# Optimization experiments

Hardware: AMD Instinct MI355X
Metric: run time of the kernel (lower is better)

Reference implementation:

```python
import jax, jax.numpy as jnp
import numpy as np

EPS = 1e-5
CHUNK = 256
N_LAYERS = 4
D_MODEL = 1024
D_INNER = 2048
D_HEAD = 64
N_HEADS = 32
D_STATE = 64
D_CONV = 4
CONV_DIM = D_INNER + 2 * D_STATE  # ngroups=1
D_IN_PROJ = 2 * D_INNER + 2 * D_STATE + N_HEADS


def silu(x):
    return x * jax.nn.sigmoid(x)


def rmsnorm(x, w):
    return x * jax.lax.rsqrt(jnp.mean(x * x, axis=-1, keepdims=True) + EPS) * w


def segsum(x):
    # x: [..., T] -> [..., T, T] lower-triangular segment sums, -inf above diag
    T = x.shape[-1]
    cs = jnp.cumsum(x, axis=-1)
    ss = cs[..., :, None] - cs[..., None, :]
    mask = jnp.tril(jnp.ones((T, T), dtype=bool))
    return jnp.where(mask, ss, -jnp.inf)


def ssd(X, A, B, C, chunk):
    # X: [b,l,h,p] (already scaled by dt), A: [b,l,h] (= dt * A_head), B,C: [b,l,n] (ngroups=1)
    b, l, h, p = X.shape
    c = l // chunk
    X = X.reshape(b, c, chunk, h, p)
    A = A.reshape(b, c, chunk, h).transpose(0, 3, 1, 2)  # [b,h,c,l]
    B = B.reshape(b, c, chunk, -1)
    C = C.reshape(b, c, chunk, -1)
    Acs = jnp.cumsum(A, axis=-1)  # [b,h,c,l]
    # intra-chunk (diagonal blocks)
    Lm = jnp.exp(segsum(A))  # [b,h,c,l,l]
    Y_diag = jnp.einsum('bcln,bcsn,bhcls,bcshp->bclhp', C, B, Lm, X)
    # chunk end states
    decay_states = jnp.exp(Acs[..., -1:] - Acs)  # [b,h,c,l]
    states = jnp.einsum('bcln,bhcl,bclhp->bchpn', B, decay_states, X)
    # inter-chunk recurrence (c is small -> dense segsum over chunks)
    A_last = jnp.pad(Acs[..., -1], ((0, 0), (0, 0), (1, 0)))  # [b,h,c+1]
    decay_chunk = jnp.exp(segsum(A_last))  # [b,h,c+1,c+1]
    states = jnp.concatenate([jnp.zeros_like(states[:, :1]), states], axis=1)
    new_states = jnp.einsum('bhzc,bchpn->bzhpn', decay_chunk, states)
    states = new_states[:, :-1]  # state entering each chunk
    Y_off = jnp.einsum('bcln,bchpn,bhcl->bclhp', C, states, jnp.exp(Acs))
    return (Y_diag + Y_off).reshape(b, l, h, p)


def mamba2_layer(x, in_w, conv_w, conv_b, dt_bias, A_log, D, gnorm_w, out_w):
    b, l, _ = x.shape
    zxbcdt = jnp.einsum('bld,ed->ble', x, in_w)  # [b,l,D_IN_PROJ]
    z = zxbcdt[..., :D_INNER]
    xBC = zxbcdt[..., D_INNER:D_INNER + CONV_DIM]
    dt = zxbcdt[..., D_INNER + CONV_DIM:]  # [b,l,h]
    # depthwise causal conv1d + silu
    xpad = jnp.pad(xBC, ((0, 0), (D_CONV - 1, 0), (0, 0)))
    xconv = conv_b
    for k in range(D_CONV):
        xconv = xconv + xpad[:, k:k + l, :] * conv_w[:, k]
    xBC = silu(xconv)
    x_in = xBC[..., :D_INNER]
    B = xBC[..., D_INNER:D_INNER + D_STATE]
    C = xBC[..., D_INNER + D_STATE:]
    dt = jax.nn.softplus(dt + dt_bias)  # [b,l,h]
    A = -jnp.exp(A_log)  # [h]
    X = x_in.reshape(b, l, N_HEADS, D_HEAD)
    y = ssd(X * dt[..., None], dt * A, B, C, CHUNK)
    y = y + D[None, None, :, None] * X
    y = y.reshape(b, l, D_INNER)
    y = rmsnorm(y * silu(z), gnorm_w)
    return jnp.einsum('ble,de->bld', y, out_w)


def setup_inputs() -> dict:
    key = jax.random.key(0)
    ks = jax.random.split(key, 8)
    x = jax.random.normal(ks[0], (2, 2048, D_MODEL), dtype=jnp.float32)
    in_proj_w = jax.random.normal(ks[1], (N_LAYERS, D_IN_PROJ, D_MODEL), dtype=jnp.float32) * 0.02
    conv_w = jax.random.uniform(ks[2], (N_LAYERS, CONV_DIM, D_CONV), dtype=jnp.float32, minval=-0.5, maxval=0.5)
    conv_b = jnp.zeros((N_LAYERS, CONV_DIM), dtype=jnp.float32)
    A_log = jnp.log(jax.random.uniform(ks[3], (N_LAYERS, N_HEADS), dtype=jnp.float32, minval=1.0, maxval=16.0))
    dt0 = jax.random.uniform(ks[4], (N_LAYERS, N_HEADS), dtype=jnp.float32, minval=0.001, maxval=0.1)
    dt_bias = dt0 + jnp.log(-jnp.expm1(-dt0))  # inverse softplus
    D = jnp.ones((N_LAYERS, N_HEADS), dtype=jnp.float32)
    gnorm_w = jnp.ones((N_LAYERS, D_INNER), dtype=jnp.float32)
    out_proj_w = jax.random.normal(ks[5], (N_LAYERS, D_MODEL, D_INNER), dtype=jnp.float32) * 0.02
    rms_w = jnp.ones((N_LAYERS, D_MODEL), dtype=jnp.float32)
    return {"x": x, "in_proj_w": in_proj_w, "conv_w": conv_w, "conv_b": conv_b,
            "dt_bias": dt_bias, "A_log": A_log, "D": D, "gnorm_w": gnorm_w,
            "out_proj_w": out_proj_w, "rms_w": rms_w}


def reference(x, in_proj_w, conv_w, conv_b, dt_bias, A_log, D, gnorm_w, out_proj_w, rms_w):
    for i in range(N_LAYERS):
        x = x + mamba2_layer(rmsnorm(x, rms_w[i]), in_proj_w[i], conv_w[i], conv_b[i],
                             dt_bias[i], A_log[i], D[i], gnorm_w[i], out_proj_w[i])
    return x
```

## Files before the change

### kernel.cpp

```cpp
#include <hip/hip_runtime.h>
#include <cmath>

#define BATCH 2
#define LSEQ 2048
#define DMODEL 1024
#define DINNER 2048
#define NHEADS 32
#define DHEAD 64
#define DSTATE 64
#define DCONV 4
#define CONVDIM (DINNER + 2*DSTATE)
#define DINPROJ (2*DINNER + 2*DSTATE + NHEADS)
#define DINPROJ_PAD 4352
#define CHUNKSZ 256
#define NCHUNK (LSEQ/CHUNKSZ)
#define MROWS (BATCH*LSEQ)
#define EPSF 1e-5f

typedef __attribute__((ext_vector_type(8))) short shortx8;
typedef __attribute__((ext_vector_type(4))) short shortx4;
typedef __attribute__((ext_vector_type(4))) float floatx4;

__device__ __forceinline__ ushort f2bf(float f) {
  unsigned u = __float_as_uint(f);
  unsigned r = (u + 0x7fffu + ((u >> 16) & 1u)) >> 16;
  return (ushort)r;
}
__device__ __forceinline__ float bf2f(ushort b) {
  return __uint_as_float(((unsigned)b) << 16);
}

__device__ __forceinline__ shortx8 pack8(float4 a, float4 b) {
  shortx8 r;
  r[0] = (short)f2bf(a.x); r[1] = (short)f2bf(a.y);
  r[2] = (short)f2bf(a.z); r[3] = (short)f2bf(a.w);
  r[4] = (short)f2bf(b.x); r[5] = (short)f2bf(b.y);
  r[6] = (short)f2bf(b.z); r[7] = (short)f2bf(b.w);
  return r;
}

__device__ __forceinline__ void async_load16(const void* g, void* l) {
  __builtin_amdgcn_global_load_lds(
      (const __attribute__((address_space(1))) void*)g,
      (__attribute__((address_space(3))) void*)l, 16, 0, 0);
}

__device__ __forceinline__ float block_reduce_sum_256(float v, float* sb) {
  for (int off = 32; off > 0; off >>= 1) v += __shfl_down(v, off, 64);
  int lane = threadIdx.x & 63, wid = threadIdx.x >> 6;
  if (lane == 0) sb[wid] = v;
  __syncthreads();
  return sb[0] + sb[1] + sb[2] + sb[3];
}

__global__ __launch_bounds__(256) void cvt_bf16_k(const float* __restrict__ src,
                                                  ushort* __restrict__ dst,
                                                  size_t n_src, size_t n_dst) {
  size_t i = (size_t)blockIdx.x * 256 + threadIdx.x;
  if (i >= n_dst) return;
  float v = (i < n_src) ? src[i] : 0.f;
  dst[i] = f2bf(v);
}

__global__ __launch_bounds__(256) void rmsnorm_k(const float* __restrict__ x,
                                                 const float* __restrict__ w,
                                                 ushort* __restrict__ out) {
  __shared__ float sb[4];
  int r = blockIdx.x;
  const float* xr = x + (size_t)r * DMODEL;
  ushort* orow = out + (size_t)r * DMODEL;
  float v[4]; float ssq = 0.f;
  for (int i = 0; i < 4; i++) {
    v[i] = xr[threadIdx.x + i * 256];
    ssq += v[i] * v[i];
  }
  float s = block_reduce_sum_256(ssq, sb);
  float sc = rsqrtf(s / (float)DMODEL + EPSF);
  for (int i = 0; i < 4; i++) {
    int c = threadIdx.x + i * 256;
    orow[c] = f2bf(v[i] * sc * w[c]);
  }
}

__device__ __forceinline__ void stage_tile(const ushort* __restrict__ A,
                                           const ushort* __restrict__ B,
                                           char* lb, int m0, int n0, int K, int k0,
                                           int wid, int rA, int sA) {
#pragma unroll
  for (int rd = 0; rd < 2; rd++) {
    int r = rd * 64 + rA;
    int sl = sA ^ ((r ^ (r >> 2)) & 3);
    async_load16(A + (size_t)(m0 + r) * K + (k0 + sl * 8), lb + rd * 4096 + wid * 1024);
  }
#pragma unroll
  for (int rd = 0; rd < 2; rd++) {
    int r = rd * 64 + rA;
    int sl = sA ^ ((r ^ (r >> 2)) & 3);
    async_load16(B + (size_t)(n0 + r) * K + (k0 + sl * 8), lb + 8192 + rd * 4096 + wid * 1024);
  }
}

template <int CFG>
__global__ __launch_bounds__(256, CFG == 0 ? 3 : 2) void gemm_nt_mfma_pipe(
    const ushort* __restrict__ A, const ushort* __restrict__ B,
    float* __restrict__ C, ushort* __restrict__ Cbf,
    const float* __restrict__ resid, int M, int N, int K,
    int nbx, int rw, int rh) {
  constexpr int NBUF = (CFG == 0) ? 3 : 5;
  __shared__ __align__(16) char lds[NBUF][16384];
  int tid = threadIdx.x;
  int wid = tid >> 6, lane = tid & 63;
  int quad = lane >> 4, lrow = lane & 15;

  int d = blockIdx.x;
  int xcd = d & 7, wi = d >> 3;
  int ra = nbx / rw;
  int rn = xcd % ra, rm = xcd / ra;
  int bx = rn * rw + wi % rw;
  int by = rm * rh + wi / rw;

  int m0 = by * 128, n0 = bx * 128;
  int wm = (wid >> 1) * 64, wn = (wid & 1) * 64;
  int rA = tid >> 2, sA = tid & 3;

  floatx4 acc[4][4];
#pragma unroll
  for (int i = 0; i < 4; i++)
#pragma unroll
    for (int j = 0; j < 4; j++) acc[i][j] = (floatx4){0.f, 0.f, 0.f, 0.f};

  int NT = K >> 5;
  constexpr int DEPTH = (CFG == 0) ? 2 : 3;
#pragma unroll
  for (int t = 0; t < DEPTH; t++)
    stage_tile(A, B, lds[t], m0, n0, K, t * 32, wid, rA, sA);

  int cur = 0, sb = DEPTH;
  for (int t = 0; t < NT; t++) {
    if (CFG == 1) {
      __builtin_amdgcn_sched_barrier(0);
      if (t + 3 < NT) {
        stage_tile(A, B, lds[sb], m0, n0, K, (t + 3) * 32, wid, rA, sA);
        sb = (sb == NBUF - 1) ? 0 : sb + 1;
      }
      int rem = NT - 1 - t;
      if (rem >= 3)      asm volatile("s_waitcnt vmcnt(12)" ::: "memory");
      else if (rem == 2) asm volatile("s_waitcnt vmcnt(8)" ::: "memory");
      else if (rem == 1) asm volatile("s_waitcnt vmcnt(4)" ::: "memory");
      else               asm volatile("s_waitcnt vmcnt(0)" ::: "memory");
      __builtin_amdgcn_s_barrier();
      __builtin_amdgcn_sched_barrier(0);
    } else {
      if (t < NT - 1) asm volatile("s_waitcnt vmcnt(4)" ::: "memory");
      else            asm volatile("s_waitcnt vmcnt(0)" ::: "memory");
      __builtin_amdgcn_s_barrier();
      __builtin_amdgcn_sched_barrier(0);
      if (t + 2 < NT) {
        stage_tile(A, B, lds[sb], m0, n0, K, (t + 2) * 32, wid, rA, sA);
        sb = (sb == NBUF - 1) ? 0 : sb + 1;
      }
    }

    const char* Ab = lds[cur];
    const char* Bb = Ab + 8192;
    cur = (cur == NBUF - 1) ? 0 : cur + 1;
    shortx8 af[4], bfr[4];
#pragma unroll
    for (int i = 0; i < 4; i++) {
      int r = wm + i * 16 + lrow;
      af[i] = *(const shortx8*)(Ab + r * 64 + ((quad ^ ((r ^ (r >> 2)) & 3)) << 4));
    }
#pragma unroll
    for (int j = 0; j < 4; j++) {
      int r = wn + j * 16 + lrow;
      bfr[j] = *(const shortx8*)(Bb + r * 64 + ((quad ^ ((r ^ (r >> 2)) & 3)) << 4));
    }
    __builtin_amdgcn_s_setprio(1);
#pragma unroll
    for (int i = 0; i < 4; i++)
#pragma unroll
      for (int j = 0; j < 4; j++)
        acc[i][j] = __builtin_amdgcn_mfma_f32_16x16x32_bf16(af[i], bfr[j], acc[i][j], 0, 0, 0);
    __builtin_amdgcn_s_setprio(0);
  }

  if (Cbf) {
#pragma unroll
    for (int i = 0; i < 4; i++) {
      int r0 = m0 + wm + i * 16 + quad * 4;
#pragma unroll
      for (int j = 0; j < 4; j++) {
        int n = n0 + wn + j * 16 + lrow;
        if (n < N)
#pragma unroll
          for (int r = 0; r < 4; r++)
            Cbf[(size_t)(r0 + r) * N + n] = f2bf(acc[i][j][r]);
      }
    }
  } else {
    bool hasR = (resid != nullptr);
#pragma unroll
    for (int i = 0; i < 4; i++) {
      int r0 = m0 + wm + i * 16 + quad * 4;
#pragma unroll
      for (int j = 0; j < 4; j++) {
        int n = n0 + wn + j * 16 + lrow;
        if (n < N) {
#pragma unroll
          for (int r = 0; r < 4; r++) {
            size_t idx = (size_t)(r0 + r) * N + n;
            float v = acc[i][j][r];
            if (hasR) v += resid[idx];
            C[idx] = v;
          }
        }
      }
    }
  }
}

__global__ __launch_bounds__(256) void conv_silu_v2(const ushort* __restrict__ zxbf,
                                                    const float* __restrict__ cw,
                                                    const float* __restrict__ cb,
                                                    ushort* __restrict__ xbf) {
  int r0 = blockIdx.x * 8;
  int bstart = r0 & ~(LSEQ - 1);
  int tid = threadIdx.x;
#pragma unroll
  for (int rep = 0; rep < 2; rep++) {
    int ch;
    if (rep == 0) ch = tid * 8;
    else { if (tid >= (CONVDIM - 2048) / 8) break; ch = 2048 + tid * 8; }
    float wv[8][4], bias[8];
#pragma unroll
    for (int j = 0; j < 8; j++) {
      float4 w4 = *(const float4*)(cw + (ch + j) * 4);
      wv[j][0] = w4.x; wv[j][1] = w4.y; wv[j][2] = w4.z; wv[j][3] = w4.w;
      bias[j] = cb[ch + j];
    }
    float xw[11][8];
#pragma unroll
    for (int wr = 0; wr < 11; wr++) {
      int rr = r0 - 3 + wr;
      if (rr < bstart) {
#pragma unroll
        for (int j = 0; j < 8; j++) xw[wr][j] = 0.f;
      } else {
        shortx8 v = *(const shortx8*)(zxbf + (size_t)rr * DINPROJ + DINNER + ch);
#pragma unroll
        for (int j = 0; j < 8; j++) xw[wr][j] = bf2f((ushort)v[j]);
      }
    }
#pragma unroll
    for (int o = 0; o < 8; o++) {
      shortx8 ov;
#pragma unroll
      for (int j = 0; j < 8; j++) {
        float acc = bias[j];
#pragma unroll
        for (int k = 0; k < 4; k++) acc += xw[o + k][j] * wv[j][k];
        float s = acc / (1.f + expf(-acc));
        ov[j] = (short)f2bf(s);
      }
      *(shortx8*)(xbf + (size_t)(r0 + o) * CONVDIM + ch) = ov;
    }
  }
}

__global__ __launch_bounds__(256) void cumsum_k(const ushort* __restrict__ zxbf,
                                                const float* __restrict__ dt_bias,
                                                const float* __restrict__ A_log,
                                                float* __restrict__ dt_sp,
                                                float* __restrict__ dtA_cs) {
  __shared__ float buf[256];
  int bid = blockIdx.x;
  int h = bid & 31, c = (bid >> 5) & 7, b = bid >> 8;
  int l = threadIdx.x;
  float Aneg = -expf(A_log[h]);
  int row = b * LSEQ + c * CHUNKSZ + l;
  float v = bf2f(zxbf[(size_t)row * DINPROJ + DINNER + CONVDIM + h]) + dt_bias[h];
  float dtv = (v > 20.f) ? v : log1pf(expf(v));
  dt_sp[row * 32 + h] = dtv;
  buf[l] = dtv * Aneg;
  __syncthreads();
  for (int off = 1; off < 256; off <<= 1) {
    float add = (l >= off) ? buf[l - off] : 0.f;
    __syncthreads();
    buf[l] += add;
    __syncthreads();
  }
  dtA_cs[(size_t)bid * CHUNKSZ + l] = buf[l];
}

#define ST_STRIDE 72
__global__ __launch_bounds__(256) void states_mfma(const ushort* __restrict__ xbf,
                                                   const float* __restrict__ dt_sp,
                                                   const float* __restrict__ dtA_cs,
                                                   float* __restrict__ st_raw) {
  __shared__ ushort XT[64 * ST_STRIDE];
  __shared__ ushort BT[64 * ST_STRIDE];
  __shared__ float wrow[64];
  int bid = blockIdx.x;
  int h = bid & 31, c = (bid >> 5) & 7, b = bid >> 8;
  int tid = threadIdx.x;
  int w = tid >> 6, lane = tid & 63;
  int quad = lane >> 4, lrow = lane & 15;
  int cbase = bid * CHUNKSZ;
  int rowbase = b * LSEQ + c * CHUNKSZ;
  float T = dtA_cs[cbase + CHUNKSZ - 1];
  floatx4 acc[4];
  for (int jt = 0; jt < 4; jt++) acc[jt] = (floatx4){0.f, 0.f, 0.f, 0.f};
  int half = tid & 31, srb = tid >> 5;
  for (int lt = 0; lt < 4; lt++) {
    __syncthreads();
    if (tid < 64) {
      int row = rowbase + lt * 64 + tid;
      wrow[tid] = dt_sp[row * 32 + h] * __expf(T - dtA_cs[cbase + lt * 64 + tid]);
    }
    __syncthreads();
    for (int pass = 0; pass < 8; pass++) {
      int sr = srb + pass * 8;
      int row = rowbase + lt * 64 + sr;
      uint bv = *(const uint*)(xbf + (size_t)row * CONVDIM + DINNER + 2 * half);
      uint xv = *(const uint*)(xbf + (size_t)row * CONVDIM + h * DHEAD + 2 * half);
      float wv = wrow[sr];
      BT[(2 * half) * ST_STRIDE + sr]     = (ushort)(bv & 0xffff);
      BT[(2 * half + 1) * ST_STRIDE + sr] = (ushort)(bv >> 16);
      XT[(2 * half) * ST_STRIDE + sr]     = f2bf(bf2f((ushort)(xv & 0xffff)) * wv);
      XT[(2 * half + 1) * ST_STRIDE + sr] = f2bf(bf2f((ushort)(xv >> 16)) * wv);
    }
    __syncthreads();
    for (int kk = 0; kk < 64; kk += 32) {
      shortx8 af = *(const shortx8*)&XT[(w * 16 + lrow) * ST_STRIDE + kk + quad * 8];
      for (int jt = 0; jt < 4; jt++) {
        shortx8 bf = *(const shortx8*)&BT[(jt * 16 + lrow) * ST_STRIDE + kk + quad * 8];
        acc[jt] = __builtin_amdgcn_mfma_f32_16x16x32_bf16(af, bf, acc[jt], 0, 0, 0);
      }
    }
  }
  size_t base = (size_t)bid * (DHEAD * DSTATE);
  for (int jt = 0; jt < 4; jt++) {
    int n = jt * 16 + lrow;
    for (int r = 0; r < 4; r++) {
      int p = w * 16 + quad * 4 + r;
      st_raw[base + (size_t)p * 64 + n] = acc[jt][r];
    }
  }
}

__global__ __launch_bounds__(256) void scan_k(float* __restrict__ st,
                                              const float* __restrict__ dtA_cs) {
  int bid = blockIdx.x;
  int seg = bid & 3, h = (bid >> 2) & 31, b = bid >> 7;
  int tid = threadIdx.x;
  int off = seg * 1024;
  float s[4];
  for (int i = 0; i < 4; i++) s[i] = 0.f;
  for (int c = 0; c < NCHUNK; c++) {
    int g = (b * NCHUNK + c) * 32 + h;
    float dec = expf(dtA_cs[(size_t)g * CHUNKSZ + CHUNKSZ - 1]);
    size_t base = (size_t)g * (DHEAD * DSTATE) + off;
    for (int i = 0; i < 4; i++) {
      int idx = tid + i * 256;
      float raw = st[base + idx];
      st[base + idx] = s[i];
      s[i] = s[i] * dec + raw;
    }
  }
}

#define BS_STRIDE 72
#define XT_STRIDE 68
#define PW_STRIDE 72
__global__ __launch_bounds__(256) void ydiag_mfma(const ushort* __restrict__ xbf,
                                                  const float* __restrict__ dt_sp,
                                                  const float* __restrict__ dtA_cs,
                                                  const float* __restrict__ st_in,
                                                  ushort* __restrict__ Y) {
  __shared__ ushort Bs[64 * BS_STRIDE];
  __shared__ ushort XsT[64 * XT_STRIDE];
  __shared__ ushort Pw[4 * 16 * PW_STRIDE];
  __shared__ float cs[256];
  int tid = threadIdx.x;
  int w = tid >> 6, lane = tid & 63;
  int quad = lane >> 4, lrow = lane & 15;
  int bid = blockIdx.x;
  int lt = bid & 3, h = (bid >> 2) & 31, c = (bid >> 7) & 7, b = bid >> 10;
  int g = (b * NCHUNK + c) * 32 + h;
  int cbase = g * CHUNKSZ;
  int rowbase = b * LSEQ + c * CHUNKSZ;

  cs[tid] = dtA_cs[cbase + tid];
  __syncthreads();

  int mrow = lt * 64 + w * 16;
  float csl[4];
  for (int r = 0; r < 4; r++) csl[r] = cs[mrow + quad * 4 + r];

  shortx8 Cf[2];
  {
    const ushort* cp = xbf + (size_t)(rowbase + mrow + lrow) * CONVDIM + DINNER + DSTATE;
    for (int q = 0; q < 2; q++)
      Cf[q] = *(const shortx8*)(cp + q * 32 + quad * 8);
  }

  floatx4 acc[4];
  for (int jt = 0; jt < 4; jt++) acc[jt] = (floatx4){0.f, 0.f, 0.f, 0.f};
  const float* stp = st_in + (size_t)g * (DHEAD * DSTATE);
  for (int q = 0; q < 2; q++) {
    for (int jt = 0; jt < 4; jt++) {
      const float* sp = stp + (size_t)(jt * 16 + lrow) * 64 + q * 32 + quad * 8;
      shortx8 sf = pack8(*(const float4*)sp, *(const float4*)(sp + 4));
      acc[jt] = __builtin_amdgcn_mfma_f32_16x16x32_bf16(Cf[q], sf, acc[jt], 0, 0, 0);
    }
  }
  for (int jt = 0; jt < 4; jt++)
    for (int r = 0; r < 4; r++) acc[jt][r] *= __expf(csl[r]);

  ushort* myP = Pw + w * 16 * PW_STRIDE;
  int half = tid & 31, srb = tid >> 5;
  for (int st = 0; st <= lt; st++) {
    __syncthreads();
    for (int pass = 0; pass < 8; pass++) {
      int sr = srb + pass * 8;
      int row = rowbase + st * 64 + sr;
      uint bv = *(const uint*)(xbf + (size_t)row * CONVDIM + DINNER + 2 * half);
      *(uint*)&Bs[sr * BS_STRIDE + 2 * half] = bv;
      float dtv = dt_sp[row * 32 + h];
      uint xv = *(const uint*)(xbf + (size_t)row * CONVDIM + h * DHEAD + 2 * half);
      XsT[(2 * half) * XT_STRIDE + sr]     = f2bf(bf2f((ushort)(xv & 0xffff)) * dtv);
      XsT[(2 * half + 1) * XT_STRIDE + sr] = f2bf(bf2f((ushort)(xv >> 16)) * dtv);
    }
    __syncthreads();
    for (int jt = 0; jt < 4; jt++) {
      floatx4 s = (floatx4){0.f, 0.f, 0.f, 0.f};
      for (int q = 0; q < 2; q++) {
        shortx8 bfr = *(const shortx8*)&Bs[(jt * 16 + lrow) * BS_STRIDE + q * 32 + quad * 8];
        s = __builtin_amdgcn_mfma_f32_16x16x32_bf16(Cf[q], bfr, s, 0, 0, 0);
      }
      int scol = st * 64 + jt * 16 + lrow;
      float css = cs[scol];
      for (int r = 0; r < 4; r++) {
        int l = mrow + quad * 4 + r;
        float v = (scol <= l) ? s[r] * __expf(csl[r] - css) : 0.f;
        myP[(quad * 4 + r) * PW_STRIDE + jt * 16 + lrow] = f2bf(v);
      }
    }
    shortx8 pf[2];
    for (int q = 0; q < 2; q++)
      pf[q] = *(const shortx8*)&myP[lrow * PW_STRIDE + q * 32 + quad * 8];
    for (int jt = 0; jt < 4; jt++) {
      for (int q = 0; q < 2; q++) {
        const ushort* xp = &XsT[(jt * 16 + lrow) * XT_STRIDE + q * 32 + quad * 8];
        shortx4 lo = *(const shortx4*)xp;
        shortx4 hi = *(const shortx4*)(xp + 4);
        shortx8 xf = __builtin_shufflevector(lo, hi, 0, 1, 2, 3, 4, 5, 6, 7);
        acc[jt] = __builtin_amdgcn_mfma_f32_16x16x32_bf16(pf[q], xf, acc[jt], 0, 0, 0);
      }
    }
  }
  int growb = rowbase + mrow + quad * 4;
  for (int jt = 0; jt < 4; jt++)
    for (int r = 0; r < 4; r++)
      Y[(size_t)(growb + r) * DINNER + h * DHEAD + jt * 16 + lrow] = f2bf(acc[jt][r]);
}

__global__ __launch_bounds__(256) void gatenorm_k(const ushort* __restrict__ Ybf,
                                                  const ushort* __restrict__ zxbf,
                                                  const ushort* __restrict__ xbf,
                                                  const float* __restrict__ Dvec,
                                                  const float* __restrict__ gw,
                                                  ushort* __restrict__ obf) {
  __shared__ float sb[4];
  int r = blockIdx.x;
  const ushort* yr = Ybf + (size_t)r * DINNER;
  const ushort* zr = zxbf + (size_t)r * DINPROJ;
  const ushort* xr = xbf + (size_t)r * CONVDIM;
  ushort* orow = obf + (size_t)r * DINNER;
  float t[8]; float ssq = 0.f;
  for (int i = 0; i < 8; i++) {
    int cc = threadIdx.x + i * 256;
    float z = bf2f(zr[cc]);
    float yv = bf2f(yr[cc]) + Dvec[cc >> 6] * bf2f(xr[cc]);
    float gv = yv * (z / (1.f + expf(-z)));
    t[i] = gv;
    ssq += gv * gv;
  }
  float s = block_reduce_sum_256(ssq, sb);
  float sc = rsqrtf(s / (float)DINNER + EPSF);
  for (int i = 0; i < 8; i++) {
    int cc = threadIdx.x + i * 256;
    orow[cc] = f2bf(t[i] * sc * gw[cc]);
  }
}

extern "C" void kernel_launch(void* const* d_in, const int* in_sizes, int n_in,
                              void* d_out, int out_size, void* d_ws, size_t ws_size,
                              hipStream_t stream) {
  const float* x_in     = (const float*)d_in[0];
  const float* in_w     = (const float*)d_in[1];
  const float* conv_w   = (const float*)d_in[2];
  const float* conv_b   = (const float*)d_in[3];
  const float* dt_bias  = (const float*)d_in[4];
  const float* A_log    = (const float*)d_in[5];
  const float* Dvec     = (const float*)d_in[6];
  const float* gnorm_w  = (const float*)d_in[7];
  const float* out_w    = (const float*)d_in[8];
  const float* rms_w    = (const float*)d_in[9];
  float* out = (float*)d_out;

  float* ws = (float*)d_ws;
  size_t o = 0;
  float* x_cur  = ws + o; o += (size_t)MROWS * DMODEL;
  ushort* zx_bf = (ushort*)(ws + o); o += (size_t)MROWS * DINPROJ / 2;
  ushort* xbf   = (ushort*)(ws + o); o += (size_t)MROWS * CONVDIM / 2;
  float* dt_sp  = ws + o; o += (size_t)MROWS * NHEADS;
  float* dtA_cs = ws + o; o += (size_t)BATCH * NCHUNK * NHEADS * CHUNKSZ;
  float* st     = ws + o; o += (size_t)BATCH * NCHUNK * NHEADS * DHEAD * DSTATE;
  ushort* Ybf   = (ushort*)(ws + o); o += (size_t)MROWS * DINNER / 2;
  ushort* act_bf = (ushort*)(ws + o); o += (size_t)MROWS * DINNER / 2;
  ushort* w_bf   = (ushort*)(ws + o); o += (size_t)DINPROJ_PAD * DMODEL / 2;

  hipMemcpyAsync(x_cur, x_in, (size_t)MROWS * DMODEL * sizeof(float),
                 hipMemcpyDeviceToDevice, stream);

  for (int i = 0; i < 4; i++) {
    const float* in_w_i   = in_w    + (size_t)i * DINPROJ * DMODEL;
    const float* conv_w_i = conv_w  + (size_t)i * CONVDIM * DCONV;
    const float* conv_b_i = conv_b  + (size_t)i * CONVDIM;
    const float* dtb_i    = dt_bias + (size_t)i * NHEADS;
    const float* Alog_i   = A_log   + (size_t)i * NHEADS;
    const float* D_i      = Dvec    + (size_t)i * NHEADS;
    const float* gw_i     = gnorm_w + (size_t)i * DINNER;
    const float* out_w_i  = out_w   + (size_t)i * DMODEL * DINNER;
    const float* rms_w_i  = rms_w   + (size_t)i * DMODEL;

    {
      size_t ns = (size_t)DINPROJ * DMODEL, nd = (size_t)DINPROJ_PAD * DMODEL;
      cvt_bf16_k<<<(nd + 255) / 256, 256, 0, stream>>>(in_w_i, w_bf, ns, nd);
    }
    rmsnorm_k<<<MROWS, 256, 0, stream>>>(x_cur, rms_w_i, act_bf);
    gemm_nt_mfma_pipe<0><<<(DINPROJ_PAD / 128) * (MROWS / 128), 256, 0, stream>>>(
        act_bf, w_bf, nullptr, zx_bf, nullptr, MROWS, DINPROJ, DMODEL,
        DINPROJ_PAD / 128, 17, 8);
    conv_silu_v2<<<MROWS / 8, 256, 0, stream>>>(zx_bf, conv_w_i, conv_b_i, xbf);
    cumsum_k<<<BATCH * NCHUNK * NHEADS, 256, 0, stream>>>(zx_bf, dtb_i, Alog_i, dt_sp, dtA_cs);
    states_mfma<<<BATCH * NCHUNK * NHEADS, 256, 0, stream>>>(xbf, dt_sp, dtA_cs, st);
    scan_k<<<BATCH * NHEADS * 4, 256, 0, stream>>>(st, dtA_cs);
    ydiag_mfma<<<BATCH * NCHUNK * NHEADS * 4, 256, 0, stream>>>(
        xbf, dt_sp, dtA_cs, st, Ybf);
    gatenorm_k<<<MROWS, 256, 0, stream>>>(Ybf, zx_bf, xbf, D_i, gw_i, act_bf);
    {
      size_t ns = (size_t)DMODEL * DINNER;
      cvt_bf16_k<<<(ns + 255) / 256, 256, 0, stream>>>(out_w_i, w_bf, ns, ns);
    }
    float* outC = (i == 3) ? out : x_cur;
    gemm_nt_mfma_pipe<1><<<(DMODEL / 128) * (MROWS / 128), 256, 0, stream>>>(
        act_bf, w_bf, outC, nullptr, x_cur, MROWS, DMODEL, DINNER,
        DMODEL / 128, 4, 8);
  }
}
```

Baseline: 984.2 us.

## Hoist weight conversion, merge conv and cumsum, swizzle states LDS, vectorize norms

All per-layer in_proj and out_proj weights are converted to bf16 in one launch up front when the workspace is large enough, replacing eight per-layer conversion kernels with one. The conv+silu and dt cumsum kernels are merged into a single launch whose blocks split by index. The states kernel's LDS transpose now uses an XOR swizzle to reduce bank conflicts. The rmsnorm and gatenorm kernels switch to contiguous vectorized loads and stores. The hoisted path needs extra workspace and falls back to the old per-layer conversion if the workspace is too small.

```diff
diff --git a/kernel.cpp b/kernel.cpp
--- a/kernel.cpp
+++ b/kernel.cpp
@@ -62,6 +62,27 @@
   dst[i] = f2bf(v);
 }
 
+__global__ __launch_bounds__(256) void cvt_w_all(const float* __restrict__ in_w,
+                                                 const float* __restrict__ out_w,
+                                                 ushort* __restrict__ in_bf,
+                                                 ushort* __restrict__ out_bf) {
+  unsigned i = blockIdx.x * 256u + threadIdx.x;
+  const unsigned PL = (unsigned)DINPROJ_PAD * DMODEL;
+  const unsigned n1 = 4u * PL;
+  const unsigned n2 = 4u * DMODEL * DINNER;
+  if (i < n1) {
+    unsigned layer = i / PL, rem = i % PL;
+    unsigned row = rem / DMODEL, col = rem % DMODEL;
+    float v = (row < DINPROJ)
+                  ? in_w[((size_t)layer * DINPROJ + row) * DMODEL + col]
+                  : 0.f;
+    in_bf[i] = f2bf(v);
+  } else if (i < n1 + n2) {
+    unsigned j = i - n1;
+    out_bf[j] = f2bf(out_w[j]);
+  }
+}
+
 __global__ __launch_bounds__(256) void rmsnorm_k(const float* __restrict__ x,
                                                  const float* __restrict__ w,
                                                  ushort* __restrict__ out) {
@@ -69,17 +90,18 @@
   int r = blockIdx.x;
   const float* xr = x + (size_t)r * DMODEL;
   ushort* orow = out + (size_t)r * DMODEL;
-  float v[4]; float ssq = 0.f;
-  for (int i = 0; i < 4; i++) {
-    v[i] = xr[threadIdx.x + i * 256];
-    ssq += v[i] * v[i];
-  }
+  int c0 = threadIdx.x * 4;
+  float4 v4 = *(const float4*)(xr + c0);
+  float ssq = v4.x * v4.x + v4.y * v4.y + v4.z * v4.z + v4.w * v4.w;
   float s = block_reduce_sum_256(ssq, sb);
   float sc = rsqrtf(s / (float)DMODEL + EPSF);
-  for (int i = 0; i < 4; i++) {
-    int c = threadIdx.x + i * 256;
-    orow[c] = f2bf(v[i] * sc * w[c]);
-  }
+  float4 w4 = *(const float4*)(w + c0);
+  shortx4 o;
+  o[0] = (short)f2bf(v4.x * sc * w4.x);
+  o[1] = (short)f2bf(v4.y * sc * w4.y);
+  o[2] = (short)f2bf(v4.z * sc * w4.z);
+  o[3] = (short)f2bf(v4.w * sc * w4.w);
+  *(shortx4*)(orow + c0) = o;
 }
 
 __device__ __forceinline__ void stage_tile(const ushort* __restrict__ A,
@@ -219,77 +241,77 @@
   }
 }
 
-__global__ __launch_bounds__(256) void conv_silu_v2(const ushort* __restrict__ zxbf,
-                                                    const float* __restrict__ cw,
-                                                    const float* __restrict__ cb,
-                                                    ushort* __restrict__ xbf) {
-  int r0 = blockIdx.x * 8;
-  int bstart = r0 & ~(LSEQ - 1);
+__global__ __launch_bounds__(256) void convcum_k(const ushort* __restrict__ zxbf,
+                                                 const float* __restrict__ cw,
+                                                 const float* __restrict__ cb,
+                                                 ushort* __restrict__ xbf,
+                                                 const float* __restrict__ dt_bias,
+                                                 const float* __restrict__ A_log,
+                                                 float* __restrict__ dt_sp,
+                                                 float* __restrict__ dtA_cs) {
+  __shared__ float buf[256];
   int tid = threadIdx.x;
-#pragma unroll
-  for (int rep = 0; rep < 2; rep++) {
-    int ch;
-    if (rep == 0) ch = tid * 8;
-    else { if (tid >= (CONVDIM - 2048) / 8) break; ch = 2048 + tid * 8; }
-    float wv[8][4], bias[8];
-#pragma unroll
-    for (int j = 0; j < 8; j++) {
-      float4 w4 = *(const float4*)(cw + (ch + j) * 4);
-      wv[j][0] = w4.x; wv[j][1] = w4.y; wv[j][2] = w4.z; wv[j][3] = w4.w;
-      bias[j] = cb[ch + j];
-    }
-    float xw[11][8];
-#pragma unroll
-    for (int wr = 0; wr < 11; wr++) {
-      int rr = r0 - 3 + wr;
-      if (rr < bstart) {
-#pragma unroll
-        for (int j = 0; j < 8; j++) xw[wr][j] = 0.f;
-      } else {
-        shortx8 v = *(const shortx8*)(zxbf + (size_t)rr * DINPROJ + DINNER + ch);
-#pragma unroll
-        for (int j = 0; j < 8; j++) xw[wr][j] = bf2f((ushort)v[j]);
-      }
-    }
-#pragma unroll
-    for (int o = 0; o < 8; o++) {
-      shortx8 ov;
+  if (blockIdx.x < MROWS / 8) {
+    int r0 = blockIdx.x * 8;
+    int bstart = r0 & ~(LSEQ - 1);
+#pragma unroll
+    for (int rep = 0; rep < 2; rep++) {
+      int ch;
+      if (rep == 0) ch = tid * 8;
+      else { if (tid >= (CONVDIM - 2048) / 8) break; ch = 2048 + tid * 8; }
+      float wv[8][4], bias[8];
 #pragma unroll
       for (int j = 0; j < 8; j++) {
-        float acc = bias[j];
-#pragma unroll
-        for (int k = 0; k < 4; k++) acc += xw[o + k][j] * wv[j][k];
-        float s = acc / (1.f + expf(-acc));
-        ov[j] = (short)f2bf(s);
-      }
-      *(shortx8*)(xbf + (size_t)(r0 + o) * CONVDIM + ch) = ov;
-    }
-  }
-}
-
-__global__ __launch_bounds__(256) void cumsum_k(const ushort* __restrict__ zxbf,
-                                                const float* __restrict__ dt_bias,
-                                                const float* __restrict__ A_log,
-                                                float* __restrict__ dt_sp,
-                                                float* __restrict__ dtA_cs) {
-  __shared__ float buf[256];
-  int bid = blockIdx.x;
-  int h = bid & 31, c = (bid >> 5) & 7, b = bid >> 8;
-  int l = threadIdx.x;
-  float Aneg = -expf(A_log[h]);
-  int row = b * LSEQ + c * CHUNKSZ + l;
-  float v = bf2f(zxbf[(size_t)row * DINPROJ + DINNER + CONVDIM + h]) + dt_bias[h];
-  float dtv = (v > 20.f) ? v : log1pf(expf(v));
-  dt_sp[row * 32 + h] = dtv;
-  buf[l] = dtv * Aneg;
-  __syncthreads();
-  for (int off = 1; off < 256; off <<= 1) {
-    float add = (l >= off) ? buf[l - off] : 0.f;
+        float4 w4 = *(const float4*)(cw + (ch + j) * 4);
+        wv[j][0] = w4.x; wv[j][1] = w4.y; wv[j][2] = w4.z; wv[j][3] = w4.w;
+        bias[j] = cb[ch + j];
+      }
+      float xw[11][8];
+#pragma unroll
+      for (int wr = 0; wr < 11; wr++) {
+        int rr = r0 - 3 + wr;
+        if (rr < bstart) {
+#pragma unroll
+          for (int j = 0; j < 8; j++) xw[wr][j] = 0.f;
+        } else {
+          shortx8 v = *(const shortx8*)(zxbf + (size_t)rr * DINPROJ + DINNER + ch);
+#pragma unroll
+          for (int j = 0; j < 8; j++) xw[wr][j] = bf2f((ushort)v[j]);
+        }
+      }
+#pragma unroll
+      for (int o = 0; o < 8; o++) {
+        shortx8 ov;
+#pragma unroll
+        for (int j = 0; j < 8; j++) {
+          float acc = bias[j];
+#pragma unroll
+          for (int k = 0; k < 4; k++) acc += xw[o + k][j] * wv[j][k];
+          float s = acc / (1.f + expf(-acc));
+          ov[j] = (short)f2bf(s);
+        }
+        *(shortx8*)(xbf + (size_t)(r0 + o) * CONVDIM + ch) = ov;
+      }
+    }
+  } else {
+    int bid = blockIdx.x - MROWS / 8;
+    int h = bid & 31, c = (bid >> 5) & 7, b = bid >> 8;
+    int l = tid;
+    float Aneg = -expf(A_log[h]);
+    int row = b * LSEQ + c * CHUNKSZ + l;
+    float v = bf2f(zxbf[(size_t)row * DINPROJ + DINNER + CONVDIM + h]) + dt_bias[h];
+    float dtv = (v > 20.f) ? v : log1pf(expf(v));
+    dt_sp[row * 32 + h] = dtv;
+    buf[l] = dtv * Aneg;
     __syncthreads();
-    buf[l] += add;
-    __syncthreads();
-  }
-  dtA_cs[(size_t)bid * CHUNKSZ + l] = buf[l];
+    for (int off = 1; off < 256; off <<= 1) {
+      float add = (l >= off) ? buf[l - off] : 0.f;
+      __syncthreads();
+      buf[l] += add;
+      __syncthreads();
+    }
+    dtA_cs[(size_t)bid * CHUNKSZ + l] = buf[l];
+  }
 }
 
 #define ST_STRIDE 72
@@ -311,6 +333,7 @@
   floatx4 acc[4];
   for (int jt = 0; jt < 4; jt++) acc[jt] = (floatx4){0.f, 0.f, 0.f, 0.f};
   int half = tid & 31, srb = tid >> 5;
+  int ekey = (half & 7) << 3;
   for (int lt = 0; lt < 4; lt++) {
     __syncthreads();
     if (tid < 64) {
@@ -324,16 +347,21 @@
       uint bv = *(const uint*)(xbf + (size_t)row * CONVDIM + DINNER + 2 * half);
       uint xv = *(const uint*)(xbf + (size_t)row * CONVDIM + h * DHEAD + 2 * half);
       float wv = wrow[sr];
-      BT[(2 * half) * ST_STRIDE + sr]     = (ushort)(bv & 0xffff);
-      BT[(2 * half + 1) * ST_STRIDE + sr] = (ushort)(bv >> 16);
-      XT[(2 * half) * ST_STRIDE + sr]     = f2bf(bf2f((ushort)(xv & 0xffff)) * wv);
-      XT[(2 * half + 1) * ST_STRIDE + sr] = f2bf(bf2f((ushort)(xv >> 16)) * wv);
+      int sc = sr ^ ekey;
+      BT[(2 * half) * ST_STRIDE + sc]     = (ushort)(bv & 0xffff);
+      BT[(2 * half + 1) * ST_STRIDE + sc] = (ushort)(bv >> 16);
+      XT[(2 * half) * ST_STRIDE + sc]     = f2bf(bf2f((ushort)(xv & 0xffff)) * wv);
+      XT[(2 * half + 1) * ST_STRIDE + sc] = f2bf(bf2f((ushort)(xv >> 16)) * wv);
     }
     __syncthreads();
+    int arow = w * 16 + lrow;
+    int akey = ((arow >> 1) & 7) << 3;
     for (int kk = 0; kk < 64; kk += 32) {
-      shortx8 af = *(const shortx8*)&XT[(w * 16 + lrow) * ST_STRIDE + kk + quad * 8];
+      shortx8 af = *(const shortx8*)&XT[arow * ST_STRIDE + ((kk + quad * 8) ^ akey)];
       for (int jt = 0; jt < 4; jt++) {
-        shortx8 bf = *(const shortx8*)&BT[(jt * 16 + lrow) * ST_STRIDE + kk + quad * 8];
+        int brow = jt * 16 + lrow;
+        int bkey = ((brow >> 1) & 7) << 3;
+        shortx8 bf = *(const shortx8*)&BT[brow * ST_STRIDE + ((kk + quad * 8) ^ bkey)];
         acc[jt] = __builtin_amdgcn_mfma_f32_16x16x32_bf16(af, bf, acc[jt], 0, 0, 0);
       }
     }
@@ -473,25 +501,34 @@
                                                   ushort* __restrict__ obf) {
   __shared__ float sb[4];
   int r = blockIdx.x;
+  int c0 = threadIdx.x * 8;
   const ushort* yr = Ybf + (size_t)r * DINNER;
   const ushort* zr = zxbf + (size_t)r * DINPROJ;
   const ushort* xr = xbf + (size_t)r * CONVDIM;
   ushort* orow = obf + (size_t)r * DINNER;
+  shortx8 y8 = *(const shortx8*)(yr + c0);
+  shortx8 z8 = *(const shortx8*)(zr + c0);
+  shortx8 x8 = *(const shortx8*)(xr + c0);
+  float Dv = Dvec[threadIdx.x >> 3];
   float t[8]; float ssq = 0.f;
+#pragma unroll
   for (int i = 0; i < 8; i++) {
-    int cc = threadIdx.x + i * 256;
-    float z = bf2f(zr[cc]);
-    float yv = bf2f(yr[cc]) + Dvec[cc >> 6] * bf2f(xr[cc]);
+    float z = bf2f((ushort)z8[i]);
+    float yv = bf2f((ushort)y8[i]) + Dv * bf2f((ushort)x8[i]);
     float gv = yv * (z / (1.f + expf(-z)));
     t[i] = gv;
     ssq += gv * gv;
   }
   float s = block_reduce_sum_256(ssq, sb);
   float sc = rsqrtf(s / (float)DINNER + EPSF);
-  for (int i = 0; i < 8; i++) {
-    int cc = threadIdx.x + i * 256;
-    orow[cc] = f2bf(t[i] * sc * gw[cc]);
-  }
+  float4 g0 = *(const float4*)(gw + c0);
+  float4 g1 = *(const float4*)(gw + c0 + 4);
+  shortx8 o;
+  o[0] = (short)f2bf(t[0] * sc * g0.x); o[1] = (short)f2bf(t[1] * sc * g0.y);
+  o[2] = (short)f2bf(t[2] * sc * g0.z); o[3] = (short)f2bf(t[3] * sc * g0.w);
+  o[4] = (short)f2bf(t[4] * sc * g1.x); o[5] = (short)f2bf(t[5] * sc * g1.y);
+  o[6] = (short)f2bf(t[6] * sc * g1.z); o[7] = (short)f2bf(t[7] * sc * g1.w);
+  *(shortx8*)(orow + c0) = o;
 }
 
 extern "C" void kernel_launch(void* const* d_in, const int* in_sizes, int n_in,
@@ -519,44 +556,65 @@
   float* st     = ws + o; o += (size_t)BATCH * NCHUNK * NHEADS * DHEAD * DSTATE;
   ushort* Ybf   = (ushort*)(ws + o); o += (size_t)MROWS * DINNER / 2;
   ushort* act_bf = (ushort*)(ws + o); o += (size_t)MROWS * DINNER / 2;
-  ushort* w_bf   = (ushort*)(ws + o); o += (size_t)DINPROJ_PAD * DMODEL / 2;
+  size_t base_f = o;
+
+  size_t inw_f  = (size_t)4 * DINPROJ_PAD * DMODEL / 2;
+  size_t outw_f = (size_t)4 * DMODEL * DINNER / 2;
+  bool hoist = ws_size >= (base_f + inw_f + outw_f) * sizeof(float);
+
+  ushort* in_bf_all = (ushort*)(ws + base_f);
+  ushort* out_bf_all = (ushort*)(ws + base_f + inw_f);
+  ushort* w_bf_fb = (ushort*)(ws + base_f);
 
   hipMemcpyAsync(x_cur, x_in, (size_t)MROWS * DMODEL * sizeof(float),
                  hipMemcpyDeviceToDevice, stream);
 
+  if (hoist) {
+    unsigned ntot = 4u * DINPROJ_PAD * DMODEL + 4u * DMODEL * DINNER;
+    cvt_w_all<<<(ntot + 255) / 256, 256, 0, stream>>>(in_w, out_w, in_bf_all, out_bf_all);
+  }
+
   for (int i = 0; i < 4; i++) {
-    const float* in_w_i   = in_w    + (size_t)i * DINPROJ * DMODEL;
     const float* conv_w_i = conv_w  + (size_t)i * CONVDIM * DCONV;
     const float* conv_b_i = conv_b  + (size_t)i * CONVDIM;
     const float* dtb_i    = dt_bias + (size_t)i * NHEADS;
     const float* Alog_i   = A_log   + (size_t)i * NHEADS;
     const float* D_i      = Dvec    + (size_t)i * NHEADS;
     const float* gw_i     = gnorm_w + (size_t)i * DINNER;
-    const float* out_w_i  = out_w   + (size_t)i * DMODEL * DINNER;
     const float* rms_w_i  = rms_w   + (size_t)i * DMODEL;
 
-    {
+    const ushort* w1_bf;
+    const ushort* w2_bf;
+    if (hoist) {
+      w1_bf = in_bf_all  + (size_t)i * DINPROJ_PAD * DMODEL;
+      w2_bf = out_bf_all + (size_t)i * DMODEL * DINNER;
+    } else {
       size_t ns = (size_t)DINPROJ * DMODEL, nd = (size_t)DINPROJ_PAD * DMODEL;
-      cvt_bf16_k<<<(nd + 255) / 256, 256, 0, stream>>>(in_w_i, w_bf, ns, nd);
-    }
+      cvt_bf16_k<<<(nd + 255) / 256, 256, 0, stream>>>(
+          in_w + (size_t)i * DINPROJ * DMODEL, w_bf_fb, ns, nd);
+      w1_bf = w_bf_fb;
+      w2_bf = w_bf_fb;
+    }
+
     rmsnorm_k<<<MROWS, 256, 0, stream>>>(x_cur, rms_w_i, act_bf);
     gemm_nt_mfma_pipe<0><<<(DINPROJ_PAD / 128) * (MROWS / 128), 256, 0, stream>>>(
-        act_bf, w_bf, nullptr, zx_bf, nullptr, MROWS, DINPROJ, DMODEL,
+        act_bf, w1_bf, nullptr, zx_bf, nullptr, MROWS, DINPROJ, DMODEL,
         DINPROJ_PAD / 128, 17, 8);
-    conv_silu_v2<<<MROWS / 8, 256, 0, stream>>>(zx_bf, conv_w_i, conv_b_i, xbf);
-    cumsum_k<<<BATCH * NCHUNK * NHEADS, 256, 0, stream>>>(zx_bf, dtb_i, Alog_i, dt_sp, dtA_cs);
+    convcum_k<<<MROWS / 8 + BATCH * NCHUNK * NHEADS, 256, 0, stream>>>(
+        zx_bf, conv_w_i, conv_b_i, xbf, dtb_i, Alog_i, dt_sp, dtA_cs);
     states_mfma<<<BATCH * NCHUNK * NHEADS, 256, 0, stream>>>(xbf, dt_sp, dtA_cs, st);
     scan_k<<<BATCH * NHEADS * 4, 256, 0, stream>>>(st, dtA_cs);
     ydiag_mfma<<<BATCH * NCHUNK * NHEADS * 4, 256, 0, stream>>>(
         xbf, dt_sp, dtA_cs, st, Ybf);
     gatenorm_k<<<MROWS, 256, 0, stream>>>(Ybf, zx_bf, xbf, D_i, gw_i, act_bf);
-    {
+    if (!hoist) {
       size_t ns = (size_t)DMODEL * DINNER;
-      cvt_bf16_k<<<(ns + 255) / 256, 256, 0, stream>>>(out_w_i, w_bf, ns, ns);
+      cvt_bf16_k<<<(ns + 255) / 256, 256, 0, stream>>>(
+          out_w + (size_t)i * DMODEL * DINNER, (ushort*)w_bf_fb, ns, ns);
     }
     float* outC = (i == 3) ? out : x_cur;
     gemm_nt_mfma_pipe<1><<<(DMODEL / 128) * (MROWS / 128), 256, 0, stream>>>(
-        act_bf, w_bf, outC, nullptr, x_cur, MROWS, DMODEL, DINNER,
+        act_bf, w2_bf, outC, nullptr, x_cur, MROWS, DMODEL, DINNER,
         DMODEL / 128, 4, 8);
   }
 }
```

Result: faster. 921.3 us (-6.4%).
